# Optimization experiments

Measured on AMD Instinct MI355X. Metric: run time of the kernel, lower is better.

Reference implementation:

```python
import jax, jax.numpy as jnp
import numpy as np

RADIUS = 0.22
NB = 25


def fps(points, n_samples):
    """Farthest point sampling. points: [N,3] -> indices [n_samples]."""
    N = points.shape[0]

    def step(carry, _):
        mind, last = carry
        d = jnp.sum((points - points[last]) ** 2, axis=-1)  # [N]
        mind = jnp.minimum(mind, d)
        nxt = jnp.argmax(mind)
        return (mind, nxt), nxt

    init = (jnp.full((N,), jnp.inf, points.dtype), jnp.argmax(jnp.zeros((N,), points.dtype)) * 0)
    _, idxs = jax.lax.scan(step, init, None, length=n_samples - 1)
    return jnp.concatenate([jnp.zeros((1,), idxs.dtype), idxs])


def ball_knn(points, samples, radius, k):
    """For each sample, the k nearest points within `radius` (padded with the
    nearest valid neighbor, which always exists since the sample itself is in
    points with distance 0). Returns int indices [S, k]."""
    d2 = jnp.sum((samples[:, None, :] - points[None, :, :]) ** 2, axis=-1)  # [S,N]
    d2 = jnp.where(d2 <= radius * radius, d2, jnp.inf)
    neg, idx = jax.lax.top_k(-d2, k)  # ascending distance order
    valid = neg > -jnp.inf
    return jnp.where(valid, idx, idx[:, :1])


def setup_inputs() -> dict:
    key = jax.random.key(0)
    ks = jax.random.split(key, 8)
    N = 65536
    f1, f2, f3 = 80, 40, 20

    def w(k, shape):
        fan_in = shape[0]
        return jax.random.normal(k, shape, jnp.float32) * np.float32(np.sqrt(2.0 / fan_in))

    return {
        "points": jax.random.uniform(ks[0], (N, 3), jnp.float32),
        "enc_w1": w(ks[1], (3, f1)), "enc_b1": jnp.zeros((f1,), jnp.float32),
        "enc_w2": w(ks[2], (f1, f2)), "enc_b2": jnp.zeros((f2,), jnp.float32),
        "enc_w3": w(ks[3], (f2, f3)), "enc_b3": jnp.zeros((f3,), jnp.float32),
        "dec_w1": w(ks[4], (f3, f2)), "dec_b1": jnp.zeros((f2,), jnp.float32),
        "dec_w2": w(ks[5], (f2, f1)), "dec_b2": jnp.zeros((f1,), jnp.float32),
        "dec_w3": w(ks[6], (f1, NB * 3)), "dec_b3": jnp.zeros((NB * 3,), jnp.float32),
    }


def reference(points, enc_w1, enc_b1, enc_w2, enc_b2, enc_w3, enc_b3,
              dec_w1, dec_b1, dec_w2, dec_b2, dec_w3, dec_b3):
    N = points.shape[0]
    nb = dec_w3.shape[1] // 3
    n_samples = -(-N // nb)  # ceil(N * ratio), ratio = 1/nb

    # Index computations (FPS + radius query) are non-differentiable.
    p = jax.lax.stop_gradient(points)
    sample_inds = fps(p, n_samples)                    # [S]
    samples = points[sample_inds]                      # [S,3]
    rad_inds = ball_knn(p, p[sample_inds], RADIUS, nb)  # [S,nb]

    rad_cluster = jnp.repeat(jnp.arange(n_samples), nb)  # [S*nb]
    rad_points = points[rad_inds.reshape(-1)]            # [S*nb,3]
    midpoints = samples[rad_cluster]                     # [S*nb,3]
    relative = (rad_points - midpoints) / RADIUS

    # Relative autoencoder: per-point MLP -> per-cluster max pool -> decoder MLP
    h = jax.nn.relu(relative @ enc_w1 + enc_b1)
    h = jax.nn.relu(h @ enc_w2 + enc_b2)
    h = jax.nn.relu(h @ enc_w3 + enc_b3)
    feat = jnp.max(h.reshape(n_samples, nb, -1), axis=1)  # [S,f3] (mean=False)

    g = jax.nn.relu(feat @ dec_w1 + dec_b1)
    g = jax.nn.relu(g @ dec_w2 + dec_b2)
    g = g @ dec_w3 + dec_b3                              # [S, nb*3]
    relative_out = g.reshape(-1, 3)                      # [S*nb,3]

    dec_abs = relative_out * RADIUS + midpoints
    resized_deco = dec_abs.reshape(-1, nb, 3)            # [S,nb,3]
    return rad_points, rad_cluster, resized_deco
```

## Files before the change

### kernel.cpp

```cpp
#include <hip/hip_runtime.h>

typedef unsigned int u32;
typedef unsigned long long u64;

#define N_PTS 65536
#define NB_ 25
#define NSAMP 2622
#define FPS_BLOCKS 16
#define FPS_THREADS 1024
#define FPS_TOTAL (FPS_BLOCKS*FPS_THREADS)
#define PPT (N_PTS/FPS_TOTAL)
#define SLOT_STRIDE 16
#define RING_U64 (4*FPS_BLOCKS*SLOT_STRIDE)
#define CAND_CAP 7900

static_assert(FPS_TOTAL*PPT == N_PTS, "fps partition");

__device__ __forceinline__ float dist2_exact(float px,float py,float pz,
                                             float qx,float qy,float qz){
  float dx=__fsub_rn(px,qx), dy=__fsub_rn(py,qy), dz=__fsub_rn(pz,qz);
  return __fadd_rn(__fadd_rn(__fmul_rn(dx,dx),__fmul_rn(dy,dy)),__fmul_rn(dz,dz));
}

__device__ __forceinline__ u64 ald(const u64* p){
  return __hip_atomic_load(p, __ATOMIC_RELAXED, __HIP_MEMORY_SCOPE_AGENT);
}
__device__ __forceinline__ void ast(u64* p, u64 v){
  __hip_atomic_store(p, v, __ATOMIC_RELAXED, __HIP_MEMORY_SCOPE_AGENT);
}

__global__ void k_setup(const float* __restrict__ pts, float* __restrict__ xs,
                        float* __restrict__ ys, float* __restrict__ zs,
                        u32* __restrict__ sample_inds, u64* __restrict__ ring){
  int i = blockIdx.x*blockDim.x + threadIdx.x;
  if (i < N_PTS){ xs[i]=pts[3*i]; ys[i]=pts[3*i+1]; zs[i]=pts[3*i+2]; }
  if (blockIdx.x==0){
    for (int j=threadIdx.x; j<RING_U64; j+=256) ring[j]=0ULL;
    if (threadIdx.x==0) sample_inds[0] = 0u;
  }
}

__global__ void __launch_bounds__(FPS_THREADS) k_fps(
    const float* __restrict__ xs, const float* __restrict__ ys,
    const float* __restrict__ zs, u32* __restrict__ sample_inds,
    u64* __restrict__ partials)
{
  __shared__ float s_q[3];
  __shared__ u64 s_wmax[FPS_THREADS/64];
  const int tid  = threadIdx.x;
  const int b    = blockIdx.x;
  const int lane = tid & 63;
  const int wv   = tid >> 6;
  const int gt   = b*FPS_THREADS + tid;

  float acc = 0.f;
  for (int j=tid; j<N_PTS; j+=FPS_THREADS) acc += xs[j]+ys[j]+zs[j];
  if (acc == -12345.678f && tid==0) sample_inds[0]=0u;

  float px[PPT],py[PPT],pz[PPT],mind[PPT];
  #pragma unroll
  for (int k=0;k<PPT;k++){
    int i = k*FPS_TOTAL + gt;
    px[k]=xs[i]; py[k]=ys[i]; pz[k]=zs[i];
    mind[k]=__builtin_huge_valf();
  }

  if (tid==0){ s_q[0]=xs[0]; s_q[1]=ys[0]; s_q[2]=zs[0]; }
  __syncthreads();

  for (int t=0; t<NSAMP-1; ++t){
    float qx=s_q[0], qy=s_q[1], qz=s_q[2];
    u64 m = 0ULL;
    #pragma unroll
    for (int k=0;k<PPT;k++){
      float d = dist2_exact(px[k],py[k],pz[k],qx,qy,qz);
      mind[k] = fminf(mind[k], d);
      u32 idx = (u32)(k*FPS_TOTAL + gt);
      u64 pk = ((u64)__float_as_uint(mind[k])<<32) | (u64)(0xFFFFFFFFu - idx);
      m = (pk>m)?pk:m;
    }
    #pragma unroll
    for (int off=1; off<64; off<<=1){ u64 o=__shfl_xor(m,off,64); if(o>m)m=o; }
    if (lane==0) s_wmax[wv]=m;
    __syncthreads();
    if (wv==0){
      u64 wm = s_wmax[lane & (FPS_THREADS/64 - 1)];
      #pragma unroll
      for (int off=1; off<16; off<<=1){ u64 o=__shfl_xor(wm,off,64); if(o>wm)wm=o; }
      if (lane==0){
        ast(&partials[((t&3)*FPS_BLOCKS + b)*SLOT_STRIDE], wm);
        ast(&partials[(((t+2)&3)*FPS_BLOCKS + b)*SLOT_STRIDE], 0ULL);
      }
      u64* slot = &partials[((t&3)*FPS_BLOCKS + (lane & (FPS_BLOCKS-1)))*SLOT_STRIDE];
      u64 v;
      do { v = ald(slot); }
      while (v==0ULL);
      #pragma unroll
      for (int off=1; off<16; off<<=1){ u64 o=__shfl_xor(v,off,64); if(o>v)v=o; }
      u32 widx = 0xFFFFFFFFu - (u32)(v & 0xFFFFFFFFu);
      if (lane==0){
        s_q[0]=xs[widx]; s_q[1]=ys[widx]; s_q[2]=zs[widx];
        if (b==0) sample_inds[t+1]=widx;
      }
    }
    __syncthreads();
  }
}

__global__ void __launch_bounds__(256) k_ballknn(
    const float* __restrict__ xs, const float* __restrict__ ys,
    const float* __restrict__ zs, const u32* __restrict__ sample_inds,
    u32* __restrict__ rad_inds, float* __restrict__ out_pts,
    float* __restrict__ out_cluster)
{
  __shared__ u64 s_list[CAND_CAP];
  __shared__ u64 s_red[4];
  __shared__ u64 s_win;
  __shared__ u32 s_cnt, s_first;
  const int s = blockIdx.x, tid = threadIdx.x;
  const u32 si = sample_inds[s];
  const float qx=xs[si], qy=ys[si], qz=zs[si];
  const float R2 = (float)(0.22*0.22);
  if (tid==0) s_cnt=0u;
  __syncthreads();

  for (int j=tid; j<N_PTS; j+=256){
    float d2 = dist2_exact(xs[j],ys[j],zs[j],qx,qy,qz);
    if (d2 <= R2){
      u32 pos = atomicAdd(&s_cnt,1u);
      if (pos < CAND_CAP) s_list[pos] = ((u64)__float_as_uint(d2)<<32) | (u64)j;
    }
  }
  __syncthreads();
  const int n = (int)min(s_cnt,(u32)CAND_CAP);

  for (int r=0; r<NB_; ++r){
    u64 m = ~0ULL; int mpos = -1;
    for (int p=tid; p<n; p+=256){
      u64 v=s_list[p];
      if (v<m){ m=v; mpos=p; }
    }
    u64 mm=m;
    #pragma unroll
    for (int off=1; off<64; off<<=1){ u64 o=__shfl_xor(mm,off,64); if(o<mm)mm=o; }
    if ((tid&63)==0) s_red[tid>>6]=mm;
    __syncthreads();
    if (tid==0){
      u64 w=s_red[0];
      #pragma unroll
      for (int i=1;i<4;i++) if (s_red[i]<w) w=s_red[i];
      s_win=w;
      if (r==0) s_first=(u32)(w & 0xFFFFFFFFu);
    }
    __syncthreads();
    u64 w = s_win;
    if (m==w && mpos>=0) s_list[mpos]=~0ULL;
    if (tid==0){
      u32 widx = (r < n) ? (u32)(w & 0xFFFFFFFFu) : s_first;
      int o = s*NB_ + r;
      rad_inds[o]=widx;
      out_pts[o*3+0]=xs[widx]; out_pts[o*3+1]=ys[widx]; out_pts[o*3+2]=zs[widx];
      out_cluster[o]=(float)s;
    }
    __syncthreads();
  }
}

__global__ void __launch_bounds__(256) k_mlp(
    const float* __restrict__ xs, const float* __restrict__ ys,
    const float* __restrict__ zs, const u32* __restrict__ sample_inds,
    const u32* __restrict__ rad_inds,
    const float* __restrict__ ew1, const float* __restrict__ eb1,
    const float* __restrict__ ew2, const float* __restrict__ eb2,
    const float* __restrict__ ew3, const float* __restrict__ eb3,
    const float* __restrict__ dw1, const float* __restrict__ db1,
    const float* __restrict__ dw2, const float* __restrict__ db2,
    const float* __restrict__ dw3, const float* __restrict__ db3,
    float* __restrict__ out_deco)
{
  __shared__ float rel[NB_][3], mid[3];
  __shared__ float h1[NB_][80], h2[NB_][40], h3[NB_][20];
  __shared__ float feat[20], g1[40], g2[80];
  const int s=blockIdx.x, tid=threadIdx.x;

  if (tid==0){ u32 si=sample_inds[s]; mid[0]=xs[si]; mid[1]=ys[si]; mid[2]=zs[si]; }
  __syncthreads();
  if (tid < NB_){
    u32 ri = rad_inds[s*NB_+tid];
    rel[tid][0]=(xs[ri]-mid[0])/0.22f;
    rel[tid][1]=(ys[ri]-mid[1])/0.22f;
    rel[tid][2]=(zs[ri]-mid[2])/0.22f;
  }
  __syncthreads();
  for (int o=tid;o<NB_*80;o+=256){
    int p=o/80, f=o-p*80;
    float a=eb1[f]+rel[p][0]*ew1[0*80+f]+rel[p][1]*ew1[1*80+f]+rel[p][2]*ew1[2*80+f];
    h1[p][f]=fmaxf(a,0.f);
  }
  __syncthreads();
  for (int o=tid;o<NB_*40;o+=256){
    int p=o/40, f=o-p*40;
    float a=eb2[f];
    for (int k=0;k<80;k++) a += h1[p][k]*ew2[k*40+f];
    h2[p][f]=fmaxf(a,0.f);
  }
  __syncthreads();
  for (int o=tid;o<NB_*20;o+=256){
    int p=o/20, f=o-p*20;
    float a=eb3[f];
    for (int k=0;k<40;k++) a += h2[p][k]*ew3[k*20+f];
    h3[p][f]=fmaxf(a,0.f);
  }
  __syncthreads();
  if (tid<20){
    float m=h3[0][tid];
    for (int p=1;p<NB_;p++) m=fmaxf(m,h3[p][tid]);
    feat[tid]=m;
  }
  __syncthreads();
  if (tid<40){
    float a=db1[tid];
    for (int k=0;k<20;k++) a += feat[k]*dw1[k*40+tid];
    g1[tid]=fmaxf(a,0.f);
  }
  __syncthreads();
  if (tid<80){
    float a=db2[tid];
    for (int k=0;k<40;k++) a += g1[k]*dw2[k*80+tid];
    g2[tid]=fmaxf(a,0.f);
  }
  __syncthreads();
  if (tid<NB_*3){
    float a=db3[tid];
    for (int k=0;k<80;k++) a += g2[k]*dw3[k*75+tid];
    int p=tid/3, c=tid-p*3;
    out_deco[(s*NB_+p)*3+c] = a*0.22f + mid[c];
  }
}

extern "C" void kernel_launch(void* const* d_in, const int* in_sizes, int n_in,
                              void* d_out, int out_size, void* d_ws, size_t ws_size,
                              hipStream_t stream){
  const float* pts=(const float*)d_in[0];
  const float* ew1=(const float*)d_in[1];  const float* eb1=(const float*)d_in[2];
  const float* ew2=(const float*)d_in[3];  const float* eb2=(const float*)d_in[4];
  const float* ew3=(const float*)d_in[5];  const float* eb3=(const float*)d_in[6];
  const float* dw1=(const float*)d_in[7];  const float* db1=(const float*)d_in[8];
  const float* dw2=(const float*)d_in[9];  const float* db2=(const float*)d_in[10];
  const float* dw3=(const float*)d_in[11]; const float* db3=(const float*)d_in[12];

  float* out = (float*)d_out;
  float* out_pts     = out;
  float* out_cluster = out + NSAMP*NB_*3;
  float* out_deco    = out + NSAMP*NB_*4;

  char* ws = (char*)d_ws;
  float* xs = (float*)ws;
  float* ys = xs + N_PTS;
  float* zs = ys + N_PTS;
  u32* sinds    = (u32*)(zs + N_PTS);
  u64* partials = (u64*)(sinds + 4096);
  u32* rinds    = (u32*)(partials + RING_U64);

  k_setup<<<(N_PTS+255)/256, 256, 0, stream>>>(pts, xs, ys, zs, sinds, partials);
  k_fps<<<FPS_BLOCKS, FPS_THREADS, 0, stream>>>(xs, ys, zs, sinds, partials);
  k_ballknn<<<NSAMP, 256, 0, stream>>>(xs, ys, zs, sinds, rinds, out_pts, out_cluster);
  k_mlp<<<NSAMP, 256, 0, stream>>>(xs, ys, zs, sinds, rinds,
                                   ew1,eb1,ew2,eb2,ew3,eb3,
                                   dw1,db1,dw2,db2,dw3,db3, out_deco);
}
```

Measured before the change: 6.187 ms.

## Shrink FPS blocks to 256 threads, float-max argmax, pipelined spin polling

Reduces FPS block size from 1024 to 256 threads, so each thread holds 16 points and the intra-block barrier and reduction span only 4 waves. The per-point 64-bit packed max is replaced by a float max followed by a lowest-index match scan. The cross-block spin-wait now keeps several atomic loads in flight so the arrival of the other blocks' partials is seen sooner. The aim is to cut per-iteration synchronisation latency in the 2621-step serial loop, at the cost of more registers and more ALU work per thread.

```diff
diff --git a/kernel.cpp b/kernel.cpp
--- a/kernel.cpp
+++ b/kernel.cpp
@@ -7,14 +7,15 @@
 #define NB_ 25
 #define NSAMP 2622
 #define FPS_BLOCKS 16
-#define FPS_THREADS 1024
-#define FPS_TOTAL (FPS_BLOCKS*FPS_THREADS)
-#define PPT (N_PTS/FPS_TOTAL)
+#define FPS_THREADS 256
+#define FPS_WAVES (FPS_THREADS/64)
+#define FPS_TOT (FPS_BLOCKS*FPS_THREADS)
+#define PPT (N_PTS/FPS_TOT)
 #define SLOT_STRIDE 16
 #define RING_U64 (4*FPS_BLOCKS*SLOT_STRIDE)
 #define CAND_CAP 7900
 
-static_assert(FPS_TOTAL*PPT == N_PTS, "fps partition");
+static_assert(FPS_TOT*PPT == N_PTS, "fps partition");
 
 __device__ __forceinline__ float dist2_exact(float px,float py,float pz,
                                              float qx,float qy,float qz){
@@ -46,7 +47,7 @@
     u64* __restrict__ partials)
 {
   __shared__ float s_q[3];
-  __shared__ u64 s_wmax[FPS_THREADS/64];
+  __shared__ u64 s_wmax[FPS_WAVES];
   const int tid  = threadIdx.x;
   const int b    = blockIdx.x;
   const int lane = tid & 63;
@@ -60,7 +61,7 @@
   float px[PPT],py[PPT],pz[PPT],mind[PPT];
   #pragma unroll
   for (int k=0;k<PPT;k++){
-    int i = k*FPS_TOTAL + gt;
+    int i = k*FPS_TOT + gt;
     px[k]=xs[i]; py[k]=ys[i]; pz[k]=zs[i];
     mind[k]=__builtin_huge_valf();
   }
@@ -70,31 +71,43 @@
 
   for (int t=0; t<NSAMP-1; ++t){
     float qx=s_q[0], qy=s_q[1], qz=s_q[2];
-    u64 m = 0ULL;
+
+    float maxv = -1.f;
     #pragma unroll
     for (int k=0;k<PPT;k++){
       float d = dist2_exact(px[k],py[k],pz[k],qx,qy,qz);
       mind[k] = fminf(mind[k], d);
-      u32 idx = (u32)(k*FPS_TOTAL + gt);
-      u64 pk = ((u64)__float_as_uint(mind[k])<<32) | (u64)(0xFFFFFFFFu - idx);
-      m = (pk>m)?pk:m;
-    }
+      maxv = fmaxf(maxv, mind[k]);
+    }
+    u32 kidx = 0u;
+    #pragma unroll
+    for (int k=PPT-1; k>=0; --k) if (mind[k]==maxv) kidx = (u32)(k*FPS_TOT+gt);
+    u64 m = ((u64)__float_as_uint(maxv)<<32) | (u64)(0xFFFFFFFFu - kidx);
+
     #pragma unroll
     for (int off=1; off<64; off<<=1){ u64 o=__shfl_xor(m,off,64); if(o>m)m=o; }
     if (lane==0) s_wmax[wv]=m;
     __syncthreads();
+
     if (wv==0){
-      u64 wm = s_wmax[lane & (FPS_THREADS/64 - 1)];
+      u64 BK = (lane < FPS_WAVES) ? s_wmax[lane] : 0ULL;
       #pragma unroll
-      for (int off=1; off<16; off<<=1){ u64 o=__shfl_xor(wm,off,64); if(o>wm)wm=o; }
+      for (int off=1; off<64; off<<=1){ u64 o=__shfl_xor(BK,off,64); if(o>BK)BK=o; }
       if (lane==0){
-        ast(&partials[((t&3)*FPS_BLOCKS + b)*SLOT_STRIDE], wm);
+        ast(&partials[((t&3)*FPS_BLOCKS + b)*SLOT_STRIDE], BK);
         ast(&partials[(((t+2)&3)*FPS_BLOCKS + b)*SLOT_STRIDE], 0ULL);
       }
-      u64* slot = &partials[((t&3)*FPS_BLOCKS + (lane & (FPS_BLOCKS-1)))*SLOT_STRIDE];
+      u64* sl = &partials[((t&3)*FPS_BLOCKS + (lane & (FPS_BLOCKS-1)))*SLOT_STRIDE];
+      u64 a0=ald(sl), a1=ald(sl), a2=ald(sl), a3=ald(sl), a4=ald(sl), a5=ald(sl);
       u64 v;
-      do { v = ald(slot); }
-      while (v==0ULL);
+      for(;;){
+        if (a0){ v=a0; break; }  a0=ald(sl);
+        if (a1){ v=a1; break; }  a1=ald(sl);
+        if (a2){ v=a2; break; }  a2=ald(sl);
+        if (a3){ v=a3; break; }  a3=ald(sl);
+        if (a4){ v=a4; break; }  a4=ald(sl);
+        if (a5){ v=a5; break; }  a5=ald(sl);
+      }
       #pragma unroll
       for (int off=1; off<16; off<<=1){ u64 o=__shfl_xor(v,off,64); if(o>v)v=o; }
       u32 widx = 0xFFFFFFFFu - (u32)(v & 0xFFFFFFFFu);
```

Result: slower. 6.490 ms (+4.9%).
